# Kernel tuning notes

Measured on AMD Instinct MI355X. Metric: run time of the kernel, lower is better.

## Reference

```python
import jax, jax.numpy as jnp
import numpy as np
import math

B_SZ, T_LEN, DIM = 1, 1024, 1024
D_STATE, EXPAND, NUM_SCALES, CONV_K = 16, 2, 3, 4
D_INNER = EXPAND * DIM
EPS_LOG = 1e-38
LN_EPS = 1e-5


def _causal_dwconv(x, w, b):
    # x: (B,T,D), w: (D,1,K) depthwise, b: (D,). torch Conv1d(pad=K-1)[:, :, :T] == left-pad K-1 (causal).
    y = jax.lax.conv_general_dilated(
        jnp.transpose(x, (0, 2, 1)), w, window_strides=(1,),
        padding=[(CONV_K - 1, 0)], dimension_numbers=('NCH', 'OIH', 'NCH'),
        feature_group_count=w.shape[0])
    return jnp.transpose(y, (0, 2, 1)) + b


def _ssm_core(x, cw, cb, xw, dtw, dtb, Dp):
    # x: (B,T,d_inner)
    xc = jax.nn.silu(_causal_dwconv(x, cw, cb))
    proj = xc @ xw.T                               # (B,T,2*d_state)
    B_ssm, C_ssm = proj[..., :D_STATE], proj[..., D_STATE:]
    dt = jax.nn.softplus(B_ssm @ dtw.T + dtb)      # (B,T,d_inner)
    dt = jax.nn.softplus(dt)                       # selective_scan applies softplus a second time (faithful)
    A = -jnp.arange(1, D_STATE + 1, dtype=xc.dtype)  # (d_state,) == -A_init row, same for every d_inner channel
    dA = jnp.exp(dt[..., None] * A)                # (B,T,d_inner,d_state)
    dBx = dt[..., None] * B_ssm[:, :, None, :] * xc[..., None]
    log_dA = jnp.log(jnp.clip(dA, EPS_LOG))
    log_dBx = jnp.log(jnp.clip(dBx, EPS_LOG))
    # parallel_scan_cpu: h = exp(cumsum(log_dA) + logcumsumexp(log_dBx - cumsum(log_dA)))
    a_star = jnp.cumsum(log_dA, axis=1)
    h = jnp.exp(a_star + jax.lax.cumlogsumexp(log_dBx - a_star, axis=1))
    return jnp.einsum('bts,btds->btd', C_ssm, h) + Dp * xc


def _downsample(x, stride):
    if stride == 1:
        return x
    Bb, T, D = x.shape
    Tt = (T // stride) * stride
    return x[:, :Tt].reshape(Bb, Tt // stride, stride, D).mean(2)


def _upsample(x, T_out):
    # F.interpolate(mode='linear', align_corners=False)
    T_in = x.shape[1]
    if T_in == T_out:
        return x
    scale = T_in / T_out
    pos = jnp.clip((jnp.arange(T_out, dtype=jnp.float32) + 0.5) * scale - 0.5, 0.0, T_in - 1)
    lo = jnp.floor(pos).astype(jnp.int32)
    hi = jnp.minimum(lo + 1, T_in - 1)
    w = (pos - lo.astype(pos.dtype))[None, :, None]
    return x[:, lo] * (1.0 - w) + x[:, hi] * w


def _forward(x, in_proj_w, conv_w, conv_b, xproj_w, dtproj_w, dtproj_b,
             D_param, scale_weights, gate_w1, gate_w2, out_proj_w, ln_g, ln_b):
    residual = x
    xz = x @ in_proj_w.T                           # (B,T,2*d_inner)
    x_in, gate = xz[..., :D_INNER], xz[..., D_INNER:]
    outs = []
    for s in range(NUM_SCALES):
        x_s = _downsample(x_in, 2 ** s)
        y_s = _ssm_core(x_s, conv_w[s], conv_b[s], xproj_w[s], dtproj_w[s], dtproj_b[s], D_param[s])
        outs.append(_upsample(y_s, x.shape[1]))
    w = jax.nn.softmax(scale_weights)
    fused = sum(w[s] * outs[s] for s in range(NUM_SCALES))
    ctx = sum(outs) / NUM_SCALES
    gate_ctx = jax.nn.sigmoid(jax.nn.silu(ctx @ gate_w1.T) @ gate_w2.T)
    out = (fused * gate_ctx) * jax.nn.silu(gate)
    out = out @ out_proj_w.T
    y = out + residual
    mu = y.mean(-1, keepdims=True)
    var = ((y - mu) ** 2).mean(-1, keepdims=True)
    return (y - mu) / jnp.sqrt(var + LN_EPS) * ln_g + ln_b


def setup_inputs() -> dict:
    key = jax.random.key(0)
    ks = jax.random.split(key, 12)
    g = lambda k, shp, s: (jax.random.normal(k, shp, jnp.float32) * s)
    return {
        'x': g(ks[0], (B_SZ, T_LEN, DIM), 1.0),
        'in_proj_w': g(ks[1], (2 * D_INNER, DIM), DIM ** -0.5),
        'conv_w': g(ks[2], (NUM_SCALES, D_INNER, 1, CONV_K), CONV_K ** -0.5),
        'conv_b': g(ks[3], (NUM_SCALES, D_INNER), 0.02),
        'xproj_w': g(ks[4], (NUM_SCALES, 2 * D_STATE, D_INNER), D_INNER ** -0.5),
        'dtproj_w': g(ks[5], (NUM_SCALES, D_INNER, D_STATE), D_STATE ** -0.5),
        'dtproj_b': jax.random.uniform(ks[6], (NUM_SCALES, D_INNER), jnp.float32,
                                       math.log(0.001), math.log(0.1)),
        'D_param': jnp.ones((NUM_SCALES, D_INNER), jnp.float32),
        'scale_weights': jnp.ones((NUM_SCALES,), jnp.float32) / NUM_SCALES,
        'gate_w1': g(ks[7], (D_INNER // 2, D_INNER), D_INNER ** -0.5),
        'gate_w2': g(ks[8], (D_INNER, D_INNER // 2), (D_INNER // 2) ** -0.5),
        'out_proj_w': g(ks[9], (DIM, D_INNER), D_INNER ** -0.5),
        'ln_g': jnp.ones((DIM,), jnp.float32),
        'ln_b': jnp.zeros((DIM,), jnp.float32),
    }


def reference(x, in_proj_w, conv_w, conv_b, xproj_w, dtproj_w, dtproj_b,
              D_param, scale_weights, gate_w1, gate_w2, out_proj_w, ln_g, ln_b):
    return _forward(x, in_proj_w, conv_w, conv_b, xproj_w, dtproj_w, dtproj_b,
                    D_param, scale_weights, gate_w1, gate_w2, out_proj_w, ln_g, ln_b)
```

## Files before the change

### kernel.cpp

```cpp
#include <hip/hip_runtime.h>

typedef unsigned short u16;
typedef float floatx2 __attribute__((ext_vector_type(2)));
typedef float floatx4 __attribute__((ext_vector_type(4)));
typedef short shortx8 __attribute__((ext_vector_type(8)));

#define DIN 2048

__device__ __forceinline__ u16 f2bf(float f){
  unsigned u = __float_as_uint(f);
  u = (u + 0x7fffu + ((u>>16)&1u))>>16;
  return (u16)u;
}
__device__ __forceinline__ float sigf(float x){ return 1.f/(1.f+__expf(-x)); }
__device__ __forceinline__ float siluf(float x){ return x*sigf(x); }
__device__ __forceinline__ floatx2 max2(floatx2 a, floatx2 b){
  floatx2 r; r.x = fmaxf(a.x, b.x); r.y = fmaxf(a.y, b.y); return r;
}

#define OFF_WINP  0ull
#define OFF_WG1   8388608ull
#define OFF_WG2   12582912ull
#define OFF_WOP   16777216ull
#define OFF_XB    20971520ull
#define OFF_XIN   23068672ull
#define OFF_SGATE 31457280ull
#define OFF_X1    39845888ull
#define OFF_X2    44040192ull
#define OFF_XC0   46137344ull
#define OFF_XC1   54525952ull
#define OFF_FUSED 60817408ull
#define OFF_G3O   69206016ull
#define OFF_Y0    75497472ull
#define OFF_Y1    83886080ull
#define OFF_Y2    88080384ull
#define OFF_P0    90177536ull
#define OFF_P1    90308608ull
#define OFF_P2    90374144ull
#define OFF_HC    92274688ull
#define OFF_HINIT 121634816ull
#define OFF_SARR  136314880ull
#define OFF_CTXB  OFF_XC0
#define OFF_T1B   OFF_XC1
#define OFF_YPA0  OFF_Y1
#define OFF_YPA1  (OFF_XC0 + 4194304ull)

__device__ __forceinline__ void gld_lds16(const void* g, void* l){
  __builtin_amdgcn_global_load_lds((const __attribute__((address_space(1))) unsigned*)g,
                                   (__attribute__((address_space(3))) unsigned*)l, 16, 0, 0);
}

__global__ __launch_bounds__(256) void cvt_kernel(
    const float* __restrict__ s0, u16* __restrict__ d0,
    const float* __restrict__ s1, u16* __restrict__ d1)
{
  int i = (blockIdx.x*256 + threadIdx.x)*4;
  const float* s; u16* d;
  if (i < 4194304){ s=s0; d=d0; }
  else            { s=s1; d=d1; i -= 4194304; }
  const float4 v = *(const float4*)(s + i);
  ushort4 o; o.x = f2bf(v.x); o.y = f2bf(v.y); o.z = f2bf(v.z); o.w = f2bf(v.w);
  *(ushort4*)(d + i) = o;
}

template<int MODE, int BM>
__global__ __launch_bounds__(256) void gemm_bt(
    const u16* __restrict__ A, const u16* __restrict__ B,
    int N, int K, int Ks,
    float* __restrict__ out_f, float* __restrict__ out_f2, u16* __restrict__ out_b,
    const float* __restrict__ ex0f, const float* __restrict__ ex1f,
    float* __restrict__ ex0, float* __restrict__ ex1)
{
  constexpr int NI = BM/32;
  constexpr int IP = BM/64;
  __shared__ u16 smA[2][BM*32];
  __shared__ u16 smB[2][BM*32];
  const int tid  = threadIdx.x;
  const int m0   = blockIdx.y * BM;
  const int n0   = blockIdx.x * BM;
  const int wv   = tid >> 6;
  const int lane = tid & 63;
  const int mw   = (wv >> 1) * (BM/2);
  const int nw   = (wv & 1) * (BM/2);
  const int quad = lane >> 4;
  const int l16  = lane & 15;
  const int srow = tid >> 2;
  const int scol = (tid & 3) * 8;

  floatx4 acc[NI][NI];
#pragma unroll
  for (int i=0;i<NI;i++)
#pragma unroll
    for (int j=0;j<NI;j++) acc[i][j] = (floatx4)0.f;

  const int kStart = blockIdx.z * Ks;
  const int kEnd   = kStart + Ks;

  auto stage = [&](int buf, int k0){
#pragma unroll
    for (int p=0;p<IP;p++){
      gld_lds16(A + (size_t)(m0 + p*64 + srow)*K + k0 + scol, &smA[buf][p*2048 + wv*512]);
      gld_lds16(B + (size_t)(n0 + p*64 + srow)*K + k0 + scol, &smB[buf][p*2048 + wv*512]);
    }
  };

  stage(0, kStart);
  int cur = 0;
  for (int k0 = kStart; k0 < kEnd; k0 += 32) {
    __syncthreads();
    if (k0 + 32 < kEnd) stage(cur^1, k0+32);
    shortx8 af[NI], bfr[NI];
#pragma unroll
    for (int i=0;i<NI;i++){
      af[i]  = *(const shortx8*)&smA[cur][(mw + i*16 + l16)*32 + quad*8];
      bfr[i] = *(const shortx8*)&smB[cur][(nw + i*16 + l16)*32 + quad*8];
    }
#pragma unroll
    for (int i=0;i<NI;i++)
#pragma unroll
      for (int j=0;j<NI;j++)
        acc[i][j] = __builtin_amdgcn_mfma_f32_16x16x32_bf16(af[i], bfr[j], acc[i][j], 0, 0, 0);
    cur ^= 1;
  }

#pragma unroll
  for (int i=0;i<NI;i++){
    const int mb = m0 + mw + i*16 + quad*4;
#pragma unroll
    for (int j=0;j<NI;j++){
      const int n = n0 + nw + j*16 + l16;
      const floatx4 v4 = acc[i][j];
      if (MODE == 0){
        if (n < 2048){
#pragma unroll
          for (int r=0;r<4;r++) out_f[(size_t)(mb+r)*2048 + n] = v4[r];
          ex0[(size_t)(mb>>1)*2048 + n]       = 0.5f*(v4[0]+v4[1]);
          ex0[(size_t)((mb>>1)+1)*2048 + n]   = 0.5f*(v4[2]+v4[3]);
          ex1[(size_t)(mb>>2)*2048 + n]       = 0.25f*(v4[0]+v4[1]+v4[2]+v4[3]);
        } else {
#pragma unroll
          for (int r=0;r<4;r++) out_f2[(size_t)(mb+r)*2048 + (n-2048)] = siluf(v4[r]);
        }
      } else if (MODE == 2){
#pragma unroll
        for (int r=0;r<4;r++){
          const size_t idx = (size_t)(mb+r)*N + n;
          out_b[idx] = f2bf(sigf(v4[r]) * ex0f[idx] * ex1f[idx]);
        }
      } else if (MODE == 3){
#pragma unroll
        for (int r=0;r<4;r++){
          const size_t idx = (size_t)(mb+r)*N + n;
          out_b[idx] = f2bf(siluf(v4[r]));
        }
      } else {
        float* dst = blockIdx.z ? out_f2 : out_f;
#pragma unroll
        for (int r=0;r<4;r++) dst[(size_t)(mb+r)*N + n] = v4[r];
      }
    }
  }
}

__global__ __launch_bounds__(256) void xproj_kernel(const float* __restrict__ x0,
    const float* __restrict__ x1, const float* __restrict__ x2,
    const float* __restrict__ cw, const float* __restrict__ cb,
    const float* __restrict__ xw,
    float* __restrict__ p0, float* __restrict__ p1, float* __restrict__ p2,
    const float* __restrict__ gw1c, u16* __restrict__ wG1o,
    const float* __restrict__ gw2c, u16* __restrict__ wG2o,
    const float* __restrict__ opwc, u16* __restrict__ wOpo){
  __shared__ float srow[DIN];
  if (blockIdx.x >= 1792){
    int i = (int)(blockIdx.x - 1792)*1024 + threadIdx.x*4;
    const float* sp; u16* dp;
    if (i < 2097152)      { sp=gw1c; dp=wG1o; }
    else if (i < 4194304) { sp=gw2c; dp=wG2o; i-=2097152; }
    else                  { sp=opwc; dp=wOpo; i-=4194304; }
    const float4 v = *(const float4*)(sp + i);
    ushort4 o; o.x = f2bf(v.x); o.y = f2bf(v.y); o.z = f2bf(v.z); o.w = f2bf(v.w);
    *(ushort4*)(dp + i) = o;
    return;
  }
  const int b = blockIdx.x;
  const float* xs; float* proj; int s, t;
  if (b < 1024)      { s=0; t=b;       xs=x0; proj=p0; }
  else if (b < 1536) { s=1; t=b-1024;  xs=x1; proj=p1; }
  else               { s=2; t=b-1536;  xs=x2; proj=p2; }
  const int tid = threadIdx.x;
#pragma unroll
  for (int q=0;q<2;q++){
    const int k = (q*256 + tid)*4;
    float4 xv[4];
#pragma unroll
    for (int j=0;j<4;j++){
      const int tt = t - 3 + j;
      if (tt >= 0) xv[j] = *(const float4*)(xs + (size_t)tt*DIN + k);
      else { xv[j].x = 0.f; xv[j].y = 0.f; xv[j].z = 0.f; xv[j].w = 0.f; }
    }
    const float4 w0 = *(const float4*)(cw + ((size_t)(s*DIN) + k + 0)*4);
    const float4 w1 = *(const float4*)(cw + ((size_t)(s*DIN) + k + 1)*4);
    const float4 w2 = *(const float4*)(cw + ((size_t)(s*DIN) + k + 2)*4);
    const float4 w3 = *(const float4*)(cw + ((size_t)(s*DIN) + k + 3)*4);
    const float4 cb4 = *(const float4*)(cb + (size_t)(s*DIN) + k);
    float4 r;
    r.x = siluf(cb4.x + w0.x*xv[0].x + w0.y*xv[1].x + w0.z*xv[2].x + w0.w*xv[3].x);
    r.y = siluf(cb4.y + w1.x*xv[0].y + w1.y*xv[1].y + w1.z*xv[2].y + w1.w*xv[3].y);
    r.z = siluf(cb4.z + w2.x*xv[0].z + w2.y*xv[1].z + w2.z*xv[2].z + w2.w*xv[3].z);
    r.w = siluf(cb4.w + w3.x*xv[0].w + w3.y*xv[1].w + w3.z*xv[2].w + w3.w*xv[3].w);
    *(float4*)&srow[k] = r;
  }
  __syncthreads();
  const int i = tid >> 3;
  const int j = tid & 7;
  const float4* w4 = (const float4*)(xw + ((size_t)s*32 + i)*DIN);
  const float4* s4 = (const float4*)srow;
  float acc = 0.f;
#pragma unroll 8
  for (int c=0;c<64;c++){
    const float4 sv = s4[j + 8*c];
    const float4 wv = w4[j + 8*c];
    acc += sv.x*wv.x + sv.y*wv.y + sv.z*wv.z + sv.w*wv.w;
  }
  acc += __shfl_xor(acc,1); acc += __shfl_xor(acc,2); acc += __shfl_xor(acc,4);
  if (j == 0) proj[t*32 + i] = acc;
}

__global__ __launch_bounds__(128) void scan_p1(
    const float* __restrict__ x0, const float* __restrict__ x1, const float* __restrict__ x2,
    const float* __restrict__ p0, const float* __restrict__ p1, const float* __restrict__ p2,
    const float* __restrict__ cw, const float* __restrict__ cb,
    const float* __restrict__ dtw, const float* __restrict__ dtb,
    float* __restrict__ Sarr, float* __restrict__ Hc)
{
  __shared__ float sproj[16*32];
  int b = blockIdx.x;
  const float *xs, *proj; int base, s;
  if (b < 1024)      { xs=x0; proj=p0; base=0;  s=0; }
  else if (b < 1536) { b-=1024; xs=x1; proj=p1; base=64; s=1; }
  else               { b-=1536; xs=x2; proj=p2; base=96; s=2; }
  const int chunk = b >> 4;
  const int tid   = threadIdx.x;
  const int d     = (b & 15)*128 + tid;
  const int t0    = chunk*16;
  {
    const int k = tid*4;
    *(float4*)&sproj[k] = *(const float4*)&proj[t0*32 + k];
  }
  __syncthreads();

  const float4 wc  = *(const float4*)(cw + ((size_t)(s*DIN) + d)*4);
  const float  cbv = cb[s*DIN + d];
  floatx2 w2[8];
  const floatx2* wr = (const floatx2*)(dtw + ((size_t)(s*DIN) + d)*16);
#pragma unroll
  for (int k=0;k<8;k++) w2[k] = wr[k];
  const float bias = dtb[s*DIN + d];
  const floatx2 eps2 = {1e-38f, 1e-38f};

  floatx2 H2[8];
#pragma unroll
  for (int k=0;k<8;k++) H2[k] = (floatx2)0.f;
  float S = 0.f;
  const float* xp = xs + d;
  float h0=0.f, h1=0.f, h2=0.f;
  if (chunk){
    h0 = xp[(size_t)(t0-3)*DIN];
    h1 = xp[(size_t)(t0-2)*DIN];
    h2 = xp[(size_t)(t0-1)*DIN];
  }
  for (int tt=0; tt<16; tt++){
    const float xv  = xp[(size_t)(t0+tt)*DIN];
    const float xcv = siluf(cbv + wc.x*h0 + wc.y*h1 + wc.z*h2 + wc.w*xv);
    h0=h1; h1=h2; h2=xv;
    const floatx2* Bp2 = (const floatx2*)&sproj[tt*32];
    floatx2 zz = (floatx2)0.f;
#pragma unroll
    for (int k=0;k<8;k++) zz += Bp2[k]*w2[k];
    float z = fminf(zz.x + zz.y + bias, 60.f);
    const float E     = __expf(z);
    const float denom = 2.f + E;
    const float e     = __builtin_amdgcn_rcpf(denom);
    const float dtv   = __logf(denom);
    S += dtv;
    const floatx2 c2  = {dtv*xcv, dtv*xcv};
    const floatx2 es  = {e*e, e*e};
    floatx2 ep2 = {e, e*e};
#pragma unroll
    for (int k=0;k<8;k++){
      const floatx2 dA  = max2(ep2, eps2);
      const floatx2 dBx = max2(c2*Bp2[k], eps2);
      H2[k] = dA*H2[k] + dBx;
      ep2 *= es;
    }
  }
  Sarr[(size_t)(base+chunk)*2048 + d] = S;
  float* o = Hc + (size_t)(base+chunk)*32768 + d;
#pragma unroll
  for (int k=0;k<8;k++){
    o[(size_t)(2*k  )*2048] = H2[k].x;
    o[(size_t)(2*k+1)*2048] = H2[k].y;
  }
}

__global__ __launch_bounds__(256) void scan_combine(const float* __restrict__ Sarr,
    const float* __restrict__ Hc, float* __restrict__ Hinit){
  int id = blockIdx.x*256 + threadIdx.x;
  int base, C;
  if (id < 32768)      { base=0;  C=64; }
  else if (id < 65536) { id-=32768; base=64; C=32; }
  else                 { id-=65536; base=96; C=16; }
  const int n = id >> 11, d = id & 2047;
  const float fn = -(float)(n+1);
  const size_t off = (size_t)base*32768 + id;
  const float* hc = Hc + off;
  float* hi = Hinit + off;
  const float* sp = Sarr + (size_t)base*2048 + d;
  float H = 0.f;
  for (int c=0;c<C;c++){
    hi[(size_t)c*32768] = H;
    const float e = __expf(fn * sp[(size_t)c*2048]);
    H = e*H + hc[(size_t)c*32768];
  }
}

__global__ __launch_bounds__(128) void scan_p2(
    const float* __restrict__ x0, const float* __restrict__ x1, const float* __restrict__ x2,
    const float* __restrict__ p0, const float* __restrict__ p1, const float* __restrict__ p2,
    const float* __restrict__ cw, const float* __restrict__ cb,
    const float* __restrict__ dtw, const float* __restrict__ dtb,
    const float* __restrict__ Hinit, const float* __restrict__ Dp_all,
    float* __restrict__ y0, float* __restrict__ y1, float* __restrict__ y2)
{
  __shared__ float sproj[16*32];
  int b = blockIdx.x;
  const float *xs, *proj; float* y; int base, s;
  if (b < 1024)      { xs=x0; proj=p0; y=y0; base=0;  s=0; }
  else if (b < 1536) { b-=1024; xs=x1; proj=p1; y=y1; base=64; s=1; }
  else               { b-=1536; xs=x2; proj=p2; y=y2; base=96; s=2; }
  const int chunk = b >> 4;
  const int tid   = threadIdx.x;
  const int d     = (b & 15)*128 + tid;
  const int t0    = chunk*16;
  {
    const int k = tid*4;
    *(float4*)&sproj[k] = *(const float4*)&proj[t0*32 + k];
  }
  __syncthreads();

  const float4 wc  = *(const float4*)(cw + ((size_t)(s*DIN) + d)*4);
  const float  cbv = cb[s*DIN + d];
  floatx2 w2[8];
  const floatx2* wr = (const floatx2*)(dtw + ((size_t)(s*DIN) + d)*16);
#pragma unroll
  for (int k=0;k<8;k++) w2[k] = wr[k];
  const float bias = dtb[s*DIN + d];

  floatx2 H2[8];
  const float* hi = Hinit + (size_t)(base+chunk)*32768 + d;
#pragma unroll
  for (int k=0;k<8;k++){
    H2[k].x = hi[(size_t)(2*k  )*2048];
    H2[k].y = hi[(size_t)(2*k+1)*2048];
  }
  const float Dv = Dp_all[s*DIN + d];
  const floatx2 eps2 = {1e-38f, 1e-38f};
  const float* xp = xs + d;
  float* yp = y + (size_t)t0*DIN + d;
  float h0=0.f, h1=0.f, h2=0.f;
  if (chunk){
    h0 = xp[(size_t)(t0-3)*DIN];
    h1 = xp[(size_t)(t0-2)*DIN];
    h2 = xp[(size_t)(t0-1)*DIN];
  }
  for (int tt=0; tt<16; tt++){
    const float xv  = xp[(size_t)(t0+tt)*DIN];
    const float xcv = siluf(cbv + wc.x*h0 + wc.y*h1 + wc.z*h2 + wc.w*xv);
    h0=h1; h1=h2; h2=xv;
    const floatx2* Bp2 = (const floatx2*)&sproj[tt*32];
    floatx2 zz = (floatx2)0.f;
#pragma unroll
    for (int k=0;k<8;k++) zz += Bp2[k]*w2[k];
    float z = fminf(zz.x + zz.y + bias, 60.f);
    const float E     = __expf(z);
    const float denom = 2.f + E;
    const float e     = __builtin_amdgcn_rcpf(denom);
    const float dtv   = __logf(denom);
    const floatx2 c2 = {dtv*xcv, dtv*xcv};
    const floatx2 es = {e*e, e*e};
    floatx2 ep2 = {e, e*e};
    floatx2 pacc2 = (floatx2)0.f;
#pragma unroll
    for (int k=0;k<8;k++){
      const floatx2 dA  = max2(ep2, eps2);
      const floatx2 dBx = max2(c2*Bp2[k], eps2);
      H2[k] = dA*H2[k] + dBx;
      pacc2 += Bp2[8+k]*H2[k];
      ep2 *= es;
    }
    yp[(size_t)tt*DIN] = pacc2.x + pacc2.y + Dv*xcv;
  }
}

__device__ __forceinline__ float ups_read(const float* __restrict__ ys, int Tin, int t, int d){
  const float scale = (float)Tin * (1.f/1024.f);
  float pos = ((float)t + 0.5f)*scale - 0.5f;
  pos = fminf(fmaxf(pos, 0.f), (float)(Tin-1));
  const int lo = (int)floorf(pos);
  const float w = pos - (float)lo;
  const int hi = min(lo+1, Tin-1);
  return ys[(size_t)lo*DIN + d]*(1.f-w) + ys[(size_t)hi*DIN + d]*w;
}

__global__ __launch_bounds__(256) void fuse_kernel(const float* __restrict__ y0,
    const float* __restrict__ y1, const float* __restrict__ y2,
    const float* __restrict__ sw, u16* __restrict__ ctxb, float* __restrict__ fused){
  const int idx = blockIdx.x*256 + threadIdx.x;
  const int t = idx >> 11, d = idx & 2047;
  const float w0r = sw[0], w1r = sw[1], w2r = sw[2];
  const float mx = fmaxf(w0r, fmaxf(w1r, w2r));
  float e0 = __expf(w0r-mx), e1 = __expf(w1r-mx), e2 = __expf(w2r-mx);
  const float inv = 1.f/(e0+e1+e2);
  e0 *= inv; e1 *= inv; e2 *= inv;
  const float o0 = y0[idx];
  const float o1 = ups_read(y1, 512, t, d);
  const float o2 = ups_read(y2, 256, t, d);
  fused[idx] = e0*o0 + e1*o1 + e2*o2;
  ctxb[idx]  = f2bf((o0+o1+o2)*(1.f/3.f));
}

__global__ __launch_bounds__(256) void ln_kernel(const float* __restrict__ ya,
    const float* __restrict__ yb, const float* __restrict__ xr,
    const float* __restrict__ g, const float* __restrict__ b, float* __restrict__ out){
  __shared__ float red[4];
  const int t = blockIdx.x;
  const size_t ro = (size_t)t*1024;
  float v[4];
  float s = 0.f;
#pragma unroll
  for (int i=0;i<4;i++){
    const int c = threadIdx.x + i*256;
    v[i] = ya[ro+c] + yb[ro+c] + xr[ro+c];
    s += v[i];
  }
  s += __shfl_xor(s,1); s += __shfl_xor(s,2); s += __shfl_xor(s,4);
  s += __shfl_xor(s,8); s += __shfl_xor(s,16); s += __shfl_xor(s,32);
  if ((threadIdx.x & 63) == 0) red[threadIdx.x>>6] = s;
  __syncthreads();
  const float mu = (red[0]+red[1]+red[2]+red[3]) * (1.f/1024.f);
  __syncthreads();
  float q = 0.f;
#pragma unroll
  for (int i=0;i<4;i++){ const float dd = v[i]-mu; q += dd*dd; }
  q += __shfl_xor(q,1); q += __shfl_xor(q,2); q += __shfl_xor(q,4);
  q += __shfl_xor(q,8); q += __shfl_xor(q,16); q += __shfl_xor(q,32);
  if ((threadIdx.x & 63) == 0) red[threadIdx.x>>6] = q;
  __syncthreads();
  const float rstd = rsqrtf((red[0]+red[1]+red[2]+red[3]) * (1.f/1024.f) + 1e-5f);
#pragma unroll
  for (int i=0;i<4;i++){
    const int c = threadIdx.x + i*256;
    out[ro + c] = (v[i]-mu)*rstd*g[c] + b[c];
  }
}

extern "C" void kernel_launch(void* const* d_in, const int* in_sizes, int n_in,
                              void* d_out, int out_size, void* d_ws, size_t ws_size,
                              hipStream_t stream) {
  const float* x     = (const float*)d_in[0];
  const float* inpw  = (const float*)d_in[1];
  const float* convw = (const float*)d_in[2];
  const float* convb = (const float*)d_in[3];
  const float* xpw   = (const float*)d_in[4];
  const float* dtw   = (const float*)d_in[5];
  const float* dtb   = (const float*)d_in[6];
  const float* Dp    = (const float*)d_in[7];
  const float* sw    = (const float*)d_in[8];
  const float* gw1   = (const float*)d_in[9];
  const float* gw2   = (const float*)d_in[10];
  const float* opw   = (const float*)d_in[11];
  const float* lng   = (const float*)d_in[12];
  const float* lnb   = (const float*)d_in[13];
  float* out = (float*)d_out;

  char* ws = (char*)d_ws;
  u16*    wInp  = (u16*)   (ws + OFF_WINP);
  u16*    wG1   = (u16*)   (ws + OFF_WG1);
  u16*    wG2   = (u16*)   (ws + OFF_WG2);
  u16*    wOp   = (u16*)   (ws + OFF_WOP);
  u16*    xb    = (u16*)   (ws + OFF_XB);
  float*  xin   = (float*) (ws + OFF_XIN);
  float*  sgate = (float*) (ws + OFF_SGATE);
  float*  x1    = (float*) (ws + OFF_X1);
  float*  x2    = (float*) (ws + OFF_X2);
  float*  y0    = (float*) (ws + OFF_Y0);
  float*  y1    = (float*) (ws + OFF_Y1);
  float*  y2    = (float*) (ws + OFF_Y2);
  float*  p0    = (float*) (ws + OFF_P0);
  float*  p1    = (float*) (ws + OFF_P1);
  float*  p2    = (float*) (ws + OFF_P2);
  float*  Sarr  = (float*) (ws + OFF_SARR);
  float*  Hc    = (float*) (ws + OFF_HC);
  float*  Hinit = (float*) (ws + OFF_HINIT);
  u16*    ctxb  = (u16*)   (ws + OFF_CTXB);
  u16*    t1b   = (u16*)   (ws + OFF_T1B);
  float*  fused = (float*) (ws + OFF_FUSED);
  u16*    g3o   = (u16*)   (ws + OFF_G3O);
  float*  ypa0  = (float*) (ws + OFF_YPA0);
  float*  ypa1  = (float*) (ws + OFF_YPA1);

  cvt_kernel<<<5120, 256, 0, stream>>>(inpw, wInp, x, xb);
  gemm_bt<0,64><<<dim3(64, 16, 1), 256, 0, stream>>>(xb, wInp, 4096, 1024, 1024,
                                                     xin, sgate, nullptr, nullptr, nullptr, x1, x2);
  xproj_kernel<<<7936, 256, 0, stream>>>(xin, x1, x2, convw, convb, xpw, p0, p1, p2,
                                         gw1, wG1, gw2, wG2, opw, wOp);
  scan_p1<<<1792, 128, 0, stream>>>(xin, x1, x2, p0, p1, p2, convw, convb, dtw, dtb, Sarr, Hc);
  scan_combine<<<384, 256, 0, stream>>>(Sarr, Hc, Hinit);
  scan_p2<<<1792, 128, 0, stream>>>(xin, x1, x2, p0, p1, p2, convw, convb, dtw, dtb,
                                    Hinit, Dp, y0, y1, y2);
  fuse_kernel<<<(1024*DIN)/256, 256, 0, stream>>>(y0, y1, y2, sw, ctxb, fused);
  gemm_bt<3,64><<<dim3(16, 16, 1), 256, 0, stream>>>(ctxb, wG1, 1024, 2048, 2048,
                                                     nullptr, nullptr, t1b, nullptr, nullptr, nullptr, nullptr);
  gemm_bt<2,64><<<dim3(32, 16, 1), 256, 0, stream>>>(t1b, wG2, 2048, 1024, 1024,
                                                     nullptr, nullptr, g3o, fused, sgate, nullptr, nullptr);
  gemm_bt<4,64><<<dim3(16, 16, 2), 256, 0, stream>>>(g3o, wOp, 1024, 2048, 1024,
                                                     ypa0, ypa1, nullptr, nullptr, nullptr, nullptr, nullptr);
  ln_kernel<<<1024, 256, 0, stream>>>(ypa0, ypa1, x, lng, lnb, out);
}
```

Measured before the change: 284.2 us.

## Split-K the gate_w1 GEMM with atomic-counter last-block silu epilogue

The gate first GEMM (M=1024,N=1024,K=2048) moves from a 256-block single-K launch to a split-K launch across two z-slices. Each slice writes fp32 partials, and a per-tile atomic counter (zeroed in cvt_kernel) picks the second-arriving block. That block adds the other partial and applies silu with the bf16 conversion. This doubles the block count to fill the CUs better, at the cost of extra fp32 partial traffic, fences and atomics.

```diff
diff --git a/kernel.cpp b/kernel.cpp
--- a/kernel.cpp
+++ b/kernel.cpp
@@ -40,8 +40,11 @@
 #define OFF_HC    92274688ull
 #define OFF_HINIT 121634816ull
 #define OFF_SARR  136314880ull
+#define OFF_TCNT  137232384ull
 #define OFF_CTXB  OFF_XC0
 #define OFF_T1B   OFF_XC1
+#define OFF_T1A0  OFF_XIN
+#define OFF_T1A1  OFF_X1
 #define OFF_YPA0  OFF_Y1
 #define OFF_YPA1  (OFF_XC0 + 4194304ull)
 
@@ -52,8 +55,10 @@
 
 __global__ __launch_bounds__(256) void cvt_kernel(
     const float* __restrict__ s0, u16* __restrict__ d0,
-    const float* __restrict__ s1, u16* __restrict__ d1)
+    const float* __restrict__ s1, u16* __restrict__ d1,
+    unsigned* __restrict__ tcnt)
 {
+  if (blockIdx.x == 0) tcnt[threadIdx.x] = 0u;
   int i = (blockIdx.x*256 + threadIdx.x)*4;
   const float* s; u16* d;
   if (i < 4194304){ s=s0; d=d0; }
@@ -69,12 +74,14 @@
     int N, int K, int Ks,
     float* __restrict__ out_f, float* __restrict__ out_f2, u16* __restrict__ out_b,
     const float* __restrict__ ex0f, const float* __restrict__ ex1f,
-    float* __restrict__ ex0, float* __restrict__ ex1)
+    float* __restrict__ ex0, float* __restrict__ ex1,
+    unsigned* __restrict__ tcnt)
 {
   constexpr int NI = BM/32;
   constexpr int IP = BM/64;
   __shared__ u16 smA[2][BM*32];
   __shared__ u16 smB[2][BM*32];
+  __shared__ unsigned sOld;
   const int tid  = threadIdx.x;
   const int m0   = blockIdx.y * BM;
   const int n0   = blockIdx.x * BM;
@@ -123,6 +130,44 @@
     cur ^= 1;
   }
 
+  if (MODE == 5){
+    float* dst = blockIdx.z ? out_f2 : out_f;
+#pragma unroll
+    for (int i=0;i<NI;i++){
+      const int mb = m0 + mw + i*16 + quad*4;
+#pragma unroll
+      for (int j=0;j<NI;j++){
+        const int n = n0 + nw + j*16 + l16;
+        const floatx4 v4 = acc[i][j];
+#pragma unroll
+        for (int r=0;r<4;r++) dst[(size_t)(mb+r)*N + n] = v4[r];
+      }
+    }
+    __threadfence();
+    __syncthreads();
+    if (tid == 0) sOld = atomicAdd(&tcnt[blockIdx.y*gridDim.x + blockIdx.x], 1u);
+    __syncthreads();
+    if (sOld == 1){
+      __threadfence();
+      const float* part = blockIdx.z ? out_f : out_f2;
+#pragma unroll
+      for (int i=0;i<NI;i++){
+        const int mb = m0 + mw + i*16 + quad*4;
+#pragma unroll
+        for (int j=0;j<NI;j++){
+          const int n = n0 + nw + j*16 + l16;
+          const floatx4 v4 = acc[i][j];
+#pragma unroll
+          for (int r=0;r<4;r++){
+            const size_t idx = (size_t)(mb+r)*N + n;
+            out_b[idx] = f2bf(siluf(v4[r] + part[idx]));
+          }
+        }
+      }
+    }
+    return;
+  }
+
 #pragma unroll
   for (int i=0;i<NI;i++){
     const int mb = m0 + mw + i*16 + quad*4;
@@ -146,12 +191,6 @@
         for (int r=0;r<4;r++){
           const size_t idx = (size_t)(mb+r)*N + n;
           out_b[idx] = f2bf(sigf(v4[r]) * ex0f[idx] * ex1f[idx]);
-        }
-      } else if (MODE == 3){
-#pragma unroll
-        for (int r=0;r<4;r++){
-          const size_t idx = (size_t)(mb+r)*N + n;
-          out_b[idx] = f2bf(siluf(v4[r]));
         }
       } else {
         float* dst = blockIdx.z ? out_f2 : out_f;
@@ -484,34 +523,37 @@
   float* out = (float*)d_out;
 
   char* ws = (char*)d_ws;
-  u16*    wInp  = (u16*)   (ws + OFF_WINP);
-  u16*    wG1   = (u16*)   (ws + OFF_WG1);
-  u16*    wG2   = (u16*)   (ws + OFF_WG2);
-  u16*    wOp   = (u16*)   (ws + OFF_WOP);
-  u16*    xb    = (u16*)   (ws + OFF_XB);
-  float*  xin   = (float*) (ws + OFF_XIN);
-  float*  sgate = (float*) (ws + OFF_SGATE);
-  float*  x1    = (float*) (ws + OFF_X1);
-  float*  x2    = (float*) (ws + OFF_X2);
-  float*  y0    = (float*) (ws + OFF_Y0);
-  float*  y1    = (float*) (ws + OFF_Y1);
-  float*  y2    = (float*) (ws + OFF_Y2);
-  float*  p0    = (float*) (ws + OFF_P0);
-  float*  p1    = (float*) (ws + OFF_P1);
-  float*  p2    = (float*) (ws + OFF_P2);
-  float*  Sarr  = (float*) (ws + OFF_SARR);
-  float*  Hc    = (float*) (ws + OFF_HC);
-  float*  Hinit = (float*) (ws + OFF_HINIT);
-  u16*    ctxb  = (u16*)   (ws + OFF_CTXB);
-  u16*    t1b   = (u16*)   (ws + OFF_T1B);
-  float*  fused = (float*) (ws + OFF_FUSED);
-  u16*    g3o   = (u16*)   (ws + OFF_G3O);
-  float*  ypa0  = (float*) (ws + OFF_YPA0);
-  float*  ypa1  = (float*) (ws + OFF_YPA1);
-
-  cvt_kernel<<<5120, 256, 0, stream>>>(inpw, wInp, x, xb);
+  u16*      wInp  = (u16*)     (ws + OFF_WINP);
+  u16*      wG1   = (u16*)     (ws + OFF_WG1);
+  u16*      wG2   = (u16*)     (ws + OFF_WG2);
+  u16*      wOp   = (u16*)     (ws + OFF_WOP);
+  u16*      xb    = (u16*)     (ws + OFF_XB);
+  float*    xin   = (float*)   (ws + OFF_XIN);
+  float*    sgate = (float*)   (ws + OFF_SGATE);
+  float*    x1    = (float*)   (ws + OFF_X1);
+  float*    x2    = (float*)   (ws + OFF_X2);
+  float*    y0    = (float*)   (ws + OFF_Y0);
+  float*    y1    = (float*)   (ws + OFF_Y1);
+  float*    y2    = (float*)   (ws + OFF_Y2);
+  float*    p0    = (float*)   (ws + OFF_P0);
+  float*    p1    = (float*)   (ws + OFF_P1);
+  float*    p2    = (float*)   (ws + OFF_P2);
+  float*    Sarr  = (float*)   (ws + OFF_SARR);
+  float*    Hc    = (float*)   (ws + OFF_HC);
+  float*    Hinit = (float*)   (ws + OFF_HINIT);
+  u16*      ctxb  = (u16*)     (ws + OFF_CTXB);
+  u16*      t1b   = (u16*)     (ws + OFF_T1B);
+  float*    fused = (float*)   (ws + OFF_FUSED);
+  u16*      g3o   = (u16*)     (ws + OFF_G3O);
+  float*    t1a0  = (float*)   (ws + OFF_T1A0);
+  float*    t1a1  = (float*)   (ws + OFF_T1A1);
+  float*    ypa0  = (float*)   (ws + OFF_YPA0);
+  float*    ypa1  = (float*)   (ws + OFF_YPA1);
+  unsigned* tcnt  = (unsigned*)(ws + OFF_TCNT);
+
+  cvt_kernel<<<5120, 256, 0, stream>>>(inpw, wInp, x, xb, tcnt);
   gemm_bt<0,64><<<dim3(64, 16, 1), 256, 0, stream>>>(xb, wInp, 4096, 1024, 1024,
-                                                     xin, sgate, nullptr, nullptr, nullptr, x1, x2);
+                                                     xin, sgate, nullptr, nullptr, nullptr, x1, x2, nullptr);
   xproj_kernel<<<7936, 256, 0, stream>>>(xin, x1, x2, convw, convb, xpw, p0, p1, p2,
                                          gw1, wG1, gw2, wG2, opw, wOp);
   scan_p1<<<1792, 128, 0, stream>>>(xin, x1, x2, p0, p1, p2, convw, convb, dtw, dtb, Sarr, Hc);
@@ -519,11 +561,11 @@
   scan_p2<<<1792, 128, 0, stream>>>(xin, x1, x2, p0, p1, p2, convw, convb, dtw, dtb,
                                     Hinit, Dp, y0, y1, y2);
   fuse_kernel<<<(1024*DIN)/256, 256, 0, stream>>>(y0, y1, y2, sw, ctxb, fused);
-  gemm_bt<3,64><<<dim3(16, 16, 1), 256, 0, stream>>>(ctxb, wG1, 1024, 2048, 2048,
-                                                     nullptr, nullptr, t1b, nullptr, nullptr, nullptr, nullptr);
+  gemm_bt<5,64><<<dim3(16, 16, 2), 256, 0, stream>>>(ctxb, wG1, 1024, 2048, 1024,
+                                                     t1a0, t1a1, t1b, nullptr, nullptr, nullptr, nullptr, tcnt);
   gemm_bt<2,64><<<dim3(32, 16, 1), 256, 0, stream>>>(t1b, wG2, 2048, 1024, 1024,
-                                                     nullptr, nullptr, g3o, fused, sgate, nullptr, nullptr);
+                                                     nullptr, nullptr, g3o, fused, sgate, nullptr, nullptr, nullptr);
   gemm_bt<4,64><<<dim3(16, 16, 2), 256, 0, stream>>>(g3o, wOp, 1024, 2048, 1024,
-                                                     ypa0, ypa1, nullptr, nullptr, nullptr, nullptr, nullptr);
+                                                     ypa0, ypa1, nullptr, nullptr, nullptr, nullptr, nullptr, nullptr);
   ln_kernel<<<1024, 256, 0, stream>>>(ypa0, ypa1, x, lng, lnb, out);
 }
```

Result: slower. 363.5 us (+27.9%).
